# Kernel optimization log

Measured on AMD Instinct MI355X. Metric: run time of the kernel, lower is better.

The kernel has to match this reference:

```python
import jax, jax.numpy as jnp
import numpy as np
from jax import lax

B, L, M, H = 8, 16, 256, 53
HID, NH, HD = 64, 4, 16  # hidden_size, n_heads, head_dim
ACT = 15  # 3 sub-actions x 5 categories


def _lstm_last(x, Wih, Whh, bih, bhh):
    # x: [N, T, D] batch_first; torch LSTM gate order i,f,g,o. Returns last hidden [N, HID].
    N = x.shape[0]
    h0 = jnp.zeros((N, HID), x.dtype)
    c0 = jnp.zeros((N, HID), x.dtype)
    def step(carry, xt):
        h, c = carry
        g = xt @ Wih.T + bih + h @ Whh.T + bhh
        i, f, gg, o = jnp.split(g, 4, axis=-1)
        c = jax.nn.sigmoid(f) * c + jax.nn.sigmoid(i) * jnp.tanh(gg)
        h = jax.nn.sigmoid(o) * jnp.tanh(c)
        return (h, c), None
    (h, _), _ = lax.scan(step, (h0, c0), x.transpose(1, 0, 2))
    return h


def setup_inputs():
    key = jax.random.key(0)
    ks = jax.random.split(key, 32)
    rn = lambda k, sh: (jax.random.normal(k, sh, jnp.float32) * 0.05)
    Gmat = jax.random.randint(ks[3], (M, M), 0, 2)
    Gmat = Gmat.at[jnp.arange(M), jnp.arange(M)].set(1)  # self-contact so no all-masked row
    return {
        'x_actor': jax.random.normal(ks[0], (B, L, M, H), jnp.float32),
        'x_critic': jax.random.normal(ks[1], (B, L, M, H), jnp.float32),
        'action': jax.random.randint(ks[2], (B, M, 3), 0, 5),
        'Gmat': Gmat,
        'Wa': rn(ks[4], (HID, H)), 'ba': jnp.zeros((HID,), jnp.float32),
        'Wg': rn(ks[5], (HID, H)), 'bg': jnp.zeros((HID,), jnp.float32),
        'Qw': rn(ks[6], (HID, HID)), 'Kw': rn(ks[7], (HID, HID)),
        'W2': rn(ks[8], (HID, 2 * HID)), 'b2': jnp.zeros((HID,), jnp.float32),
        'Wih_a': rn(ks[9], (4 * HID, HID)), 'Whh_a': rn(ks[10], (4 * HID, HID)),
        'bih_a': jnp.zeros((4 * HID,), jnp.float32), 'bhh_a': jnp.zeros((4 * HID,), jnp.float32),
        'Wih_c': rn(ks[11], (4 * HID, HID)), 'Whh_c': rn(ks[12], (4 * HID, HID)),
        'bih_c': jnp.zeros((4 * HID,), jnp.float32), 'bhh_c': jnp.zeros((4 * HID,), jnp.float32),
        'Wma1': rn(ks[13], (HID, HID)), 'bma1': jnp.zeros((HID,), jnp.float32),
        'Wma2': rn(ks[14], (ACT, HID)), 'bma2': jnp.zeros((ACT,), jnp.float32),
        'Wmc1': rn(ks[15], (HID, HID)), 'bmc1': jnp.zeros((HID,), jnp.float32),
        'Wmc2': rn(ks[16], (1, HID)), 'bmc2': jnp.zeros((1,), jnp.float32),
    }


def reference(x_actor, x_critic, action, Gmat, Wa, ba, Wg, bg, Qw, Kw, W2, b2,
              Wih_a, Whh_a, bih_a, bhh_a, Wih_c, Whh_c, bih_c, bhh_c,
              Wma1, bma1, Wma2, bma2, Wmc1, bmc1, Wmc2, bmc2):
    Bb, Ll, Mm, Hh = x_actor.shape
    xa = x_actor.transpose(1, 0, 2, 3).reshape(Ll * Bb, Mm, Hh)
    xc = xa  # original code overwrites x_critic with x_actor (preserved)
    a_lin = xa @ Wa.T + ba                               # [LB, M, HID]
    # --- GAT (GCN2) ---
    s = xc @ Wg.T + bg                                   # [LB, M, HID]
    q = (s @ Qw).reshape(-1, Mm, NH, HD)
    k = (s @ Kw).reshape(-1, Mm, NH, HD)
    s4 = s.reshape(-1, Mm, NH, HD)
    att = jnp.einsum('blhe,bshe->bhls', q, k) / jnp.asarray(128.0, s.dtype) ** 0.5
    att = jnp.where(Gmat > 0, att, jnp.asarray(-9e15, att.dtype))
    att = jax.nn.softmax(att, axis=-1)
    s_out = jnp.einsum('bshe,bhls->blhe', s4, att).reshape(-1, Mm, NH * HD)
    c_feat = jnp.concatenate([s, s_out], axis=-1) @ W2.T + b2  # [LB, M, HID]
    # --- to sequences [B*M, L, HID] ---
    xa_seq = a_lin.reshape(Ll, Bb * Mm, HID).transpose(1, 0, 2)
    xc_seq = c_feat.reshape(Ll, Bb * Mm, HID).transpose(1, 0, 2)
    ah = _lstm_last(xa_seq, Wih_a, Whh_a, bih_a, bhh_a)          # [B*M, HID]
    ch = _lstm_last(xc_seq, Wih_c, Whh_c, bih_c, bhh_c).reshape(Bb, Mm, HID)
    logits = (jnp.tanh(ah @ Wma1.T + bma1) @ Wma2.T + bma2).reshape(Bb, Mm, 3, 5)
    logp = jax.nn.log_softmax(logits, axis=-1)
    lp = jnp.take_along_axis(logp, action[..., None], axis=-1).squeeze(-1)  # [B,M,3]
    ent = -jnp.sum(jnp.exp(logp) * logp, axis=-1)                           # [B,M,3]
    value = jnp.tanh(ch @ Wmc1.T + bmc1) @ Wmc2.T + bmc2                    # [B,M,1]
    return (action, lp.sum(-1), ent.sum(-1), value)
```

## Files before the change

### kernel.cpp

```cpp
#include <hip/hip_runtime.h>
#include <math.h>

#define B_ 8
#define L_ 16
#define M_ 256
#define H_ 53
#define HID_ 64
#define LB_ 128

typedef __attribute__((ext_vector_type(8))) short bf16x8;
typedef __attribute__((ext_vector_type(4))) float f32x4;

__device__ inline unsigned short f2bf(float f) {
  unsigned u = __builtin_bit_cast(unsigned, f);
  unsigned r = (u + 0x7FFFu + ((u >> 16) & 1u)) >> 16;
  return (unsigned short)r;
}
__device__ inline float sigm(float x) { return __builtin_amdgcn_rcpf(1.f + __expf(-x)); }
__device__ inline float ftanh(float x) { return 1.f - 2.f * __builtin_amdgcn_rcpf(1.f + __expf(2.f * x)); }

__global__ __launch_bounds__(256) void kA_lin(const float* __restrict__ x,
    const float* __restrict__ Wa, const float* __restrict__ ba,
    const float* __restrict__ Wg, const float* __restrict__ bg,
    const float* __restrict__ Qw, const float* __restrict__ Kw,
    const int* __restrict__ Gmat, const float* __restrict__ Wih_c,
    const float* __restrict__ W2, const float* __restrict__ b2,
    unsigned short* __restrict__ a_lin_bf, unsigned short* __restrict__ s_b,
    unsigned short* __restrict__ q_b, unsigned short* __restrict__ k_b,
    unsigned short* __restrict__ sT_b, unsigned short* __restrict__ Wfold_b,
    float* __restrict__ bias_fold, unsigned* __restrict__ gmask) {
  __shared__ float wa_lds[HID_ * H_];
  __shared__ float wg_lds[HID_ * H_];
  __shared__ float x_lds[16][H_];
  __shared__ float s_sh[16][HID_];
  int tid = threadIdx.x;
  int row0 = blockIdx.x * 16;
  int lbA = row0 >> 8, mA0 = row0 & 255;
  for (int i = tid; i < HID_ * H_; i += 256) { wa_lds[i] = Wa[i]; wg_lds[i] = Wg[i]; }
  for (int i = tid; i < 16 * H_; i += 256) {
    int r = i / H_, j = i - r * H_;
    int row = row0 + r;
    int lb = row >> 8, m = row & 255;
    int l = lb >> 3, b = lb & 7;
    x_lds[r][j] = x[((b * L_ + l) * M_ + m) * H_ + j];
  }
  __syncthreads();
  int lane = tid & 63, wv = tid >> 6;
  float aA[4], aS[4];
  float bav = ba[lane], bgv = bg[lane];
  #pragma unroll
  for (int ri = 0; ri < 4; ++ri) { aA[ri] = bav; aS[ri] = bgv; }
  for (int j = 0; j < H_; ++j) {
    float wa = wa_lds[lane * H_ + j];
    float wg = wg_lds[lane * H_ + j];
    #pragma unroll
    for (int ri = 0; ri < 4; ++ri) {
      float xv = x_lds[wv * 4 + ri][j];
      aA[ri] = fmaf(xv, wa, aA[ri]);
      aS[ri] = fmaf(xv, wg, aS[ri]);
    }
  }
  #pragma unroll
  for (int ri = 0; ri < 4; ++ri) {
    int row = row0 + wv * 4 + ri;
    a_lin_bf[row * HID_ + lane] = f2bf(aA[ri]);
    s_sh[wv * 4 + ri][lane] = aS[ri];
    s_b[row * HID_ + lane] = f2bf(aS[ri]);
  }
  __syncthreads();
  {
    int e = tid >> 2, m4 = tid & 3;
    ushort4 v;
    v.x = f2bf(s_sh[m4 * 4 + 0][e]);
    v.y = f2bf(s_sh[m4 * 4 + 1][e]);
    v.z = f2bf(s_sh[m4 * 4 + 2][e]);
    v.w = f2bf(s_sh[m4 * 4 + 3][e]);
    *(ushort4*)&sT_b[(lbA * 64 + e) * 256 + mA0 + m4 * 4] = v;
  }
  float aq[4] = {0.f, 0.f, 0.f, 0.f}, ak[4] = {0.f, 0.f, 0.f, 0.f};
  for (int j = 0; j < HID_; ++j) {
    float qw = Qw[j * HID_ + lane];
    float kw = Kw[j * HID_ + lane];
    #pragma unroll
    for (int ri = 0; ri < 4; ++ri) {
      float sv = s_sh[wv * 4 + ri][j];
      aq[ri] = fmaf(sv, qw, aq[ri]);
      ak[ri] = fmaf(sv, kw, ak[ri]);
    }
  }
  #pragma unroll
  for (int ri = 0; ri < 4; ++ri) {
    int row = row0 + wv * 4 + ri;
    q_b[row * HID_ + lane] = f2bf(aq[ri] * 0.08838834764831845f);
    k_b[row * HID_ + lane] = f2bf(ak[ri]);
  }
  if (blockIdx.x < 256) {
    int l = blockIdx.x;
    int gv = Gmat[l * 256 + tid];
    unsigned long long msk = __ballot(gv > 0);
    if ((tid & 63) == 0) {
      gmask[l * 8 + (tid >> 6) * 2] = (unsigned)msk;
      gmask[l * 8 + (tid >> 6) * 2 + 1] = (unsigned)(msk >> 32);
    }
  } else if (blockIdx.x < 512) {
    int n = blockIdx.x - 256;
    if (tid < 128) {
      float acc = 0.f;
      for (int e = 0; e < 64; ++e) acc = fmaf(Wih_c[n * 64 + e], W2[e * 128 + tid], acc);
      Wfold_b[n * 128 + tid] = f2bf(acc);
      if (tid == 0) {
        float bacc = 0.f;
        for (int e = 0; e < 64; ++e) bacc = fmaf(Wih_c[n * 64 + e], b2[e], bacc);
        bias_fold[n] = bacc;
      }
    }
  }
}

__global__ __launch_bounds__(512, 4) void kB_attn(
    const unsigned short* __restrict__ qb, const unsigned short* __restrict__ kb,
    const unsigned short* __restrict__ sT, const unsigned* __restrict__ gmask,
    unsigned short* __restrict__ so_b) {
  int blk = blockIdx.x;
  int lb = blk >> 2;
  int l0 = (blk & 3) << 6;
  int tid = threadIdx.x;
  int lane = tid & 63, w = tid >> 6;
  int c16 = lane & 15, q4 = lane >> 4;
  int lrow0 = (w >> 1) * 16;
  int h0 = (w & 1) * 2;
  int lrow = lb * 256 + l0 + lrow0;
  int kbase = lb * 256;
  const bf16x8 z8 = {0, 0, 0, 0, 0, 0, 0, 0};
  bf16x8 bq[2];
  #pragma unroll
  for (int hp = 0; hp < 2; ++hp) {
    int h = h0 + hp;
    bq[hp] = (q4 < 2) ? *(const bf16x8*)(qb + (lrow + c16) * 64 + h * 16 + q4 * 8) : z8;
  }
  unsigned gwv[8];
  #pragma unroll
  for (int sp = 0; sp < 8; ++sp) gwv[sp] = gmask[(l0 + lrow0 + c16) * 8 + sp];
  f32x4 accO[2];
  float sumh[2];
  #pragma unroll
  for (int hp = 0; hp < 2; ++hp) { accO[hp] = (f32x4){0.f, 0.f, 0.f, 0.f}; sumh[hp] = 0.f; }

  #pragma unroll
  for (int sp = 0; sp < 8; ++sp) {
    unsigned gw = gwv[sp];
    #pragma unroll
    for (int hp = 0; hp < 2; ++hp) {
      int h = h0 + hp;
      unsigned pk0A, pk1A, pk0B, pk1B;
      #pragma unroll
      for (int tp = 0; tp < 2; ++tp) {
        int t = sp * 2 + tp;
        bf16x8 ka = z8;
        if (q4 < 2) ka = *(const bf16x8*)(kb + (kbase + t * 16 + c16) * 64 + h * 16 + q4 * 8);
        f32x4 d = __builtin_amdgcn_mfma_f32_16x16x32_bf16(ka, bq[hp], (f32x4){0.f, 0.f, 0.f, 0.f}, 0, 0, 0);
        int bitbase = tp * 16 + q4 * 4;
        float p0 = ((gw >> (bitbase + 0)) & 1u) ? __expf(d[0]) : 0.f;
        float p1 = ((gw >> (bitbase + 1)) & 1u) ? __expf(d[1]) : 0.f;
        float p2 = ((gw >> (bitbase + 2)) & 1u) ? __expf(d[2]) : 0.f;
        float p3 = ((gw >> (bitbase + 3)) & 1u) ? __expf(d[3]) : 0.f;
        sumh[hp] += (p0 + p1) + (p2 + p3);
        unsigned lo = (unsigned)f2bf(p0) | ((unsigned)f2bf(p1) << 16);
        unsigned hi = (unsigned)f2bf(p2) | ((unsigned)f2bf(p3) << 16);
        if (tp == 0) { pk0A = lo; pk1A = hi; } else { pk0B = lo; pk1B = hi; }
      }
      int srcA = ((q4 & 1) * 2) * 16 + c16, srcB = srcA + 16;
      unsigned g0A = (unsigned)__shfl((int)pk0A, srcA);
      unsigned g1A = (unsigned)__shfl((int)pk1A, srcA);
      unsigned g2A = (unsigned)__shfl((int)pk0A, srcB);
      unsigned g3A = (unsigned)__shfl((int)pk1A, srcB);
      unsigned g0B = (unsigned)__shfl((int)pk0B, srcA);
      unsigned g1B = (unsigned)__shfl((int)pk1B, srcA);
      unsigned g2B = (unsigned)__shfl((int)pk0B, srcB);
      unsigned g3B = (unsigned)__shfl((int)pk1B, srcB);
      bool useB = (q4 >= 2);
      uint4 av;
      av.x = useB ? g0B : g0A;
      av.y = useB ? g1B : g1A;
      av.z = useB ? g2B : g2A;
      av.w = useB ? g3B : g3A;
      bf16x8 af = __builtin_bit_cast(bf16x8, av);
      bf16x8 bs = *(const bf16x8*)(sT + (lb * 64 + h * 16 + c16) * 256 + sp * 32 + q4 * 8);
      accO[hp] = __builtin_amdgcn_mfma_f32_16x16x32_bf16(af, bs, accO[hp], 0, 0, 0);
    }
  }
  #pragma unroll
  for (int hp = 0; hp < 2; ++hp) {
    int h = h0 + hp;
    float s = sumh[hp];
    s += __shfl_xor(s, 16);
    s += __shfl_xor(s, 32);
    #pragma unroll
    for (int r = 0; r < 4; ++r) {
      float sv = __shfl(s, q4 * 4 + r);
      float o = accO[hp][r] / sv;
      so_b[(lb * 256 + l0 + lrow0 + q4 * 4 + r) * 64 + h * 16 + c16] = f2bf(o);
    }
  }
}

__global__ __launch_bounds__(256, 1) void kR_lstm(
    const unsigned short* __restrict__ a_lin_bf,
    const unsigned short* __restrict__ s_b, const unsigned short* __restrict__ so_b,
    const unsigned short* __restrict__ Wfold_b, const float* __restrict__ bias_fold,
    const float* __restrict__ Wih_a,
    const float* __restrict__ Whh_a, const float* __restrict__ Whh_c,
    const float* __restrict__ bih_a, const float* __restrict__ bhh_a,
    const float* __restrict__ bih_c, const float* __restrict__ bhh_c,
    const int* __restrict__ action,
    const float* __restrict__ Wma1, const float* __restrict__ bma1,
    const float* __restrict__ Wma2, const float* __restrict__ bma2,
    const float* __restrict__ Wmc1, const float* __restrict__ bmc1,
    const float* __restrict__ Wmc2, const float* __restrict__ bmc2,
    float* __restrict__ out) {
  int blk = blockIdx.x;
  int which = blk >> 7, g = blk & 127;
  int seq0 = g * 16;
  int b = seq0 >> 8, m0 = seq0 & 255;
  __shared__ __attribute__((aligned(16))) unsigned short h_lds[2][16][72];
  __shared__ __attribute__((aligned(16))) unsigned short ha_lds[16][72];
  __shared__ float logit_lds[16][16];
  __shared__ float grp_lds[16][8];
  __shared__ float val_lds[16][4];
  int tid = threadIdx.x;
  int lane = tid & 63, w = tid >> 6;
  int c16 = lane & 15, q4 = lane >> 4;
  int hs0 = w * 16;
  const float* Whh = which ? Whh_c : Whh_a;
  const float* bih = which ? bih_c : bih_a;
  const float* bhh = which ? bhh_c : bhh_a;
  bf16x8 bwhh[4][2];
  float bias[4];
  #pragma unroll
  for (int nt = 0; nt < 4; ++nt) {
    int n = nt * 64 + hs0 + c16;
    bias[nt] = bih[n] + bhh[n] + (which ? bias_fold[n] : 0.f);
    #pragma unroll
    for (int kf = 0; kf < 2; ++kf) {
      const float* wp = Whh + n * 64 + kf * 32 + q4 * 8;
      bf16x8 bb;
      #pragma unroll
      for (int j = 0; j < 8; ++j) bb[j] = (short)f2bf(wp[j]);
      bwhh[nt][kf] = bb;
    }
  }
  for (int i = tid; i < 576; i += 256) ((unsigned*)h_lds)[i] = 0u;
  float cr[4] = {0.f, 0.f, 0.f, 0.f};
  const int STEP = 2048 * 64;
  __syncthreads();
  int cur = 0;
  if (which == 0) {
    bf16x8 bwin[4][2];
    #pragma unroll
    for (int nt = 0; nt < 4; ++nt) {
      int n = nt * 64 + hs0 + c16;
      #pragma unroll
      for (int kf = 0; kf < 2; ++kf) {
        const float* wp = Wih_a + n * 64 + kf * 32 + q4 * 8;
        bf16x8 bb;
        #pragma unroll
        for (int j = 0; j < 8; ++j) bb[j] = (short)f2bf(wp[j]);
        bwin[nt][kf] = bb;
      }
    }
    const unsigned short* inb = a_lin_bf + (b * 256 + m0 + c16) * 64;
    bf16x8 i0c = *(const bf16x8*)(inb + q4 * 8);
    bf16x8 i1c = *(const bf16x8*)(inb + 32 + q4 * 8);
    for (int l = 0; l < L_; ++l) {
      bf16x8 i0n = i0c, i1n = i1c;
      if (l < L_ - 1) {
        i0n = *(const bf16x8*)(inb + (l + 1) * STEP + q4 * 8);
        i1n = *(const bf16x8*)(inb + (l + 1) * STEP + 32 + q4 * 8);
      }
      bf16x8 ah0 = *(const bf16x8*)&h_lds[cur][c16][q4 * 8];
      bf16x8 ah1 = *(const bf16x8*)&h_lds[cur][c16][32 + q4 * 8];
      f32x4 acc[4];
      #pragma unroll
      for (int nt = 0; nt < 4; ++nt) {
        f32x4 a = {bias[nt], bias[nt], bias[nt], bias[nt]};
        a = __builtin_amdgcn_mfma_f32_16x16x32_bf16(i0c, bwin[nt][0], a, 0, 0, 0);
        a = __builtin_amdgcn_mfma_f32_16x16x32_bf16(i1c, bwin[nt][1], a, 0, 0, 0);
        a = __builtin_amdgcn_mfma_f32_16x16x32_bf16(ah0, bwhh[nt][0], a, 0, 0, 0);
        a = __builtin_amdgcn_mfma_f32_16x16x32_bf16(ah1, bwhh[nt][1], a, 0, 0, 0);
        acc[nt] = a;
      }
      #pragma unroll
      for (int rr = 0; rr < 4; ++rr) {
        float si = sigm(acc[0][rr]);
        float sf = sigm(acc[1][rr]);
        float gg = ftanh(acc[2][rr]);
        float so_ = sigm(acc[3][rr]);
        cr[rr] = sf * cr[rr] + si * gg;
        float hvv = so_ * ftanh(cr[rr]);
        h_lds[cur ^ 1][q4 * 4 + rr][hs0 + c16] = f2bf(hvv);
      }
      __syncthreads();
      cur ^= 1;
      i0c = i0n; i1c = i1n;
    }
  } else {
    bf16x8 bwf[4][4];
    #pragma unroll
    for (int nt = 0; nt < 4; ++nt) {
      int n = nt * 64 + hs0 + c16;
      #pragma unroll
      for (int kc = 0; kc < 4; ++kc) {
        bwf[nt][kc] = *(const bf16x8*)(Wfold_b + n * 128 + kc * 32 + q4 * 8);
      }
    }
    const unsigned short* sbB = s_b + (b * 256 + m0 + c16) * 64;
    const unsigned short* soB = so_b + (b * 256 + m0 + c16) * 64;
    bf16x8 s0c = *(const bf16x8*)(sbB + q4 * 8);
    bf16x8 s1c = *(const bf16x8*)(sbB + 32 + q4 * 8);
    bf16x8 o0c = *(const bf16x8*)(soB + q4 * 8);
    bf16x8 o1c = *(const bf16x8*)(soB + 32 + q4 * 8);
    for (int l = 0; l < L_; ++l) {
      bf16x8 s0n = s0c, s1n = s1c, o0n = o0c, o1n = o1c;
      if (l < L_ - 1) {
        s0n = *(const bf16x8*)(sbB + (l + 1) * STEP + q4 * 8);
        s1n = *(const bf16x8*)(sbB + (l + 1) * STEP + 32 + q4 * 8);
        o0n = *(const bf16x8*)(soB + (l + 1) * STEP + q4 * 8);
        o1n = *(const bf16x8*)(soB + (l + 1) * STEP + 32 + q4 * 8);
      }
      bf16x8 ah0 = *(const bf16x8*)&h_lds[cur][c16][q4 * 8];
      bf16x8 ah1 = *(const bf16x8*)&h_lds[cur][c16][32 + q4 * 8];
      f32x4 acc[4];
      #pragma unroll
      for (int nt = 0; nt < 4; ++nt) {
        f32x4 a = {bias[nt], bias[nt], bias[nt], bias[nt]};
        a = __builtin_amdgcn_mfma_f32_16x16x32_bf16(s0c, bwf[nt][0], a, 0, 0, 0);
        a = __builtin_amdgcn_mfma_f32_16x16x32_bf16(s1c, bwf[nt][1], a, 0, 0, 0);
        a = __builtin_amdgcn_mfma_f32_16x16x32_bf16(o0c, bwf[nt][2], a, 0, 0, 0);
        a = __builtin_amdgcn_mfma_f32_16x16x32_bf16(o1c, bwf[nt][3], a, 0, 0, 0);
        a = __builtin_amdgcn_mfma_f32_16x16x32_bf16(ah0, bwhh[nt][0], a, 0, 0, 0);
        a = __builtin_amdgcn_mfma_f32_16x16x32_bf16(ah1, bwhh[nt][1], a, 0, 0, 0);
        acc[nt] = a;
      }
      #pragma unroll
      for (int rr = 0; rr < 4; ++rr) {
        float si = sigm(acc[0][rr]);
        float sf = sigm(acc[1][rr]);
        float gg = ftanh(acc[2][rr]);
        float so_ = sigm(acc[3][rr]);
        cr[rr] = sf * cr[rr] + si * gg;
        float hvv = so_ * ftanh(cr[rr]);
        h_lds[cur ^ 1][q4 * 4 + rr][hs0 + c16] = f2bf(hvv);
      }
      __syncthreads();
      cur ^= 1;
      s0c = s0n; s1c = s1n; o0c = o0n; o1c = o1n;
    }
  }
  bf16x8 fh0 = *(const bf16x8*)&h_lds[cur][c16][q4 * 8];
  bf16x8 fh1 = *(const bf16x8*)&h_lds[cur][c16][32 + q4 * 8];
  if (which == 0) {
    bf16x8 bm1[2];
    #pragma unroll
    for (int kf = 0; kf < 2; ++kf) {
      const float* wp = Wma1 + (hs0 + c16) * 64 + kf * 32 + q4 * 8;
      bf16x8 bb;
      #pragma unroll
      for (int j = 0; j < 8; ++j) bb[j] = (short)f2bf(wp[j]);
      bm1[kf] = bb;
    }
    float bs = bma1[hs0 + c16];
    f32x4 acc = {bs, bs, bs, bs};
    acc = __builtin_amdgcn_mfma_f32_16x16x32_bf16(fh0, bm1[0], acc, 0, 0, 0);
    acc = __builtin_amdgcn_mfma_f32_16x16x32_bf16(fh1, bm1[1], acc, 0, 0, 0);
    #pragma unroll
    for (int rr = 0; rr < 4; ++rr)
      ha_lds[q4 * 4 + rr][hs0 + c16] = f2bf(ftanh(acc[rr]));
    __syncthreads();
    if (w == 0) {
      bf16x8 af0 = *(const bf16x8*)&ha_lds[c16][q4 * 8];
      bf16x8 af1 = *(const bf16x8*)&ha_lds[c16][32 + q4 * 8];
      const bf16x8 z8 = {0, 0, 0, 0, 0, 0, 0, 0};
      bf16x8 bw2[2] = {z8, z8};
      float bs2 = 0.f;
      if (c16 < 15) {
        #pragma unroll
        for (int kf = 0; kf < 2; ++kf) {
          const float* wp = Wma2 + c16 * 64 + kf * 32 + q4 * 8;
          bf16x8 bb;
          #pragma unroll
          for (int j = 0; j < 8; ++j) bb[j] = (short)f2bf(wp[j]);
          bw2[kf] = bb;
        }
        bs2 = bma2[c16];
      }
      f32x4 acc2 = {bs2, bs2, bs2, bs2};
      acc2 = __builtin_amdgcn_mfma_f32_16x16x32_bf16(af0, bw2[0], acc2, 0, 0, 0);
      acc2 = __builtin_amdgcn_mfma_f32_16x16x32_bf16(af1, bw2[1], acc2, 0, 0, 0);
      #pragma unroll
      for (int rr = 0; rr < 4; ++rr)
        logit_lds[q4 * 4 + rr][c16] = acc2[rr];
    }
    __syncthreads();
    if (tid < 48) {
      int useq = tid & 15, t = tid >> 4;
      int n = seq0 + useq;
      float l0 = logit_lds[useq][t * 5 + 0], l1 = logit_lds[useq][t * 5 + 1];
      float l2 = logit_lds[useq][t * 5 + 2], l3 = logit_lds[useq][t * 5 + 3];
      float l4 = logit_lds[useq][t * 5 + 4];
      float mx = fmaxf(fmaxf(fmaxf(l0, l1), fmaxf(l2, l3)), l4);
      float sm = __expf(l0 - mx) + __expf(l1 - mx) + __expf(l2 - mx) +
                 __expf(l3 - mx) + __expf(l4 - mx);
      float lse = __logf(sm) + mx;
      int a = action[n * 3 + t];
      float lp0 = l0 - lse, lp1 = l1 - lse, lp2 = l2 - lse, lp3 = l3 - lse, lp4 = l4 - lse;
      float lpsel = logit_lds[useq][t * 5 + a] - lse;
      float ent = -(__expf(lp0) * lp0 + __expf(lp1) * lp1 + __expf(lp2) * lp2 +
                    __expf(lp3) * lp3 + __expf(lp4) * lp4);
      grp_lds[useq][t] = lpsel;
      grp_lds[useq][4 + t] = ent;
      out[n * 3 + t] = (float)a;
    }
    __syncthreads();
    if (tid < 16) {
      int n = seq0 + tid;
      out[6144 + n] = grp_lds[tid][0] + grp_lds[tid][1] + grp_lds[tid][2];
      out[8192 + n] = grp_lds[tid][4] + grp_lds[tid][5] + grp_lds[tid][6];
    }
  } else {
    bf16x8 bm1[2];
    #pragma unroll
    for (int kf = 0; kf < 2; ++kf) {
      const float* wp = Wmc1 + (hs0 + c16) * 64 + kf * 32 + q4 * 8;
      bf16x8 bb;
      #pragma unroll
      for (int j = 0; j < 8; ++j) bb[j] = (short)f2bf(wp[j]);
      bm1[kf] = bb;
    }
    float bs = bmc1[hs0 + c16];
    f32x4 acc = {bs, bs, bs, bs};
    acc = __builtin_amdgcn_mfma_f32_16x16x32_bf16(fh0, bm1[0], acc, 0, 0, 0);
    acc = __builtin_amdgcn_mfma_f32_16x16x32_bf16(fh1, bm1[1], acc, 0, 0, 0);
    float wv2 = Wmc2[hs0 + c16];
    float pv[4];
    #pragma unroll
    for (int rr = 0; rr < 4; ++rr) pv[rr] = ftanh(acc[rr]) * wv2;
    #pragma unroll
    for (int rr = 0; rr < 4; ++rr) {
      pv[rr] += __shfl_xor(pv[rr], 1);
      pv[rr] += __shfl_xor(pv[rr], 2);
      pv[rr] += __shfl_xor(pv[rr], 4);
      pv[rr] += __shfl_xor(pv[rr], 8);
    }
    if (c16 == 0) {
      #pragma unroll
      for (int rr = 0; rr < 4; ++rr) val_lds[q4 * 4 + rr][w] = pv[rr];
    }
    __syncthreads();
    if (tid < 16) {
      int n = seq0 + tid;
      out[10240 + n] = val_lds[tid][0] + val_lds[tid][1] + val_lds[tid][2] +
                       val_lds[tid][3] + bmc2[0];
    }
  }
}

extern "C" void kernel_launch(void* const* d_in, const int* in_sizes, int n_in,
                              void* d_out, int out_size, void* d_ws, size_t ws_size,
                              hipStream_t stream) {
  const float* x_actor = (const float*)d_in[0];
  const int* action = (const int*)d_in[2];
  const int* Gmat  = (const int*)d_in[3];
  const float* Wa = (const float*)d_in[4];  const float* ba = (const float*)d_in[5];
  const float* Wg = (const float*)d_in[6];  const float* bg = (const float*)d_in[7];
  const float* Qw = (const float*)d_in[8];  const float* Kw = (const float*)d_in[9];
  const float* W2 = (const float*)d_in[10]; const float* b2 = (const float*)d_in[11];
  const float* Wih_a = (const float*)d_in[12]; const float* Whh_a = (const float*)d_in[13];
  const float* bih_a = (const float*)d_in[14]; const float* bhh_a = (const float*)d_in[15];
  const float* Wih_c = (const float*)d_in[16]; const float* Whh_c = (const float*)d_in[17];
  const float* bih_c = (const float*)d_in[18]; const float* bhh_c = (const float*)d_in[19];
  const float* Wma1 = (const float*)d_in[20]; const float* bma1 = (const float*)d_in[21];
  const float* Wma2 = (const float*)d_in[22]; const float* bma2 = (const float*)d_in[23];
  const float* Wmc1 = (const float*)d_in[24]; const float* bmc1 = (const float*)d_in[25];
  const float* Wmc2 = (const float*)d_in[26]; const float* bmc2 = (const float*)d_in[27];

  unsigned short* us = (unsigned short*)d_ws;
  unsigned short* a_lin_bf = us;
  unsigned short* s_b  = us + 2097152;
  unsigned short* q_b  = us + 4194304;
  unsigned short* k_b  = us + 6291456;
  unsigned short* sT_b = us + 8388608;
  unsigned short* so_b = us + 10485760;
  unsigned short* Wfold_b = us + 12582912;
  float* fb = (float*)(us + 12615680);
  float* bias_fold = fb;
  unsigned* gmask = (unsigned*)(fb + 256);
  float* out = (float*)d_out;

  kA_lin<<<2048, 256, 0, stream>>>(x_actor, Wa, ba, Wg, bg, Qw, Kw,
                                   Gmat, Wih_c, W2, b2,
                                   a_lin_bf, s_b, q_b, k_b, sT_b, Wfold_b,
                                   bias_fold, gmask);
  kB_attn<<<512, 512, 0, stream>>>(q_b, k_b, sT_b, gmask, so_b);
  kR_lstm<<<256, 256, 0, stream>>>(a_lin_bf, s_b, so_b, Wfold_b, bias_fold,
                                   Wih_a, Whh_a, Whh_c, bih_a, bhh_a, bih_c, bhh_c,
                                   action, Wma1, bma1, Wma2, bma2,
                                   Wmc1, bmc1, Wmc2, bmc2, out);
}
```

Measured before the change: 79.41 us.

## Fold Q/K projections into input weights and compute linears with MFMA

Weight-only preprocessing (Wfold, the Q/K-through-Wg fold with its bias, and the Gmat bitmask) moves into a separate small kernel. The main linear kernel then computes a_lin, s, q and k directly from x with bf16 MFMA over 64-row tiles, replacing the scalar FP32 FMA loops. Staged LDS outputs are written out with vectorized stores. This removes the chained s→q/k matmul and the scalar FLOP cost, but adds a kernel launch and extra bf16 rounding of x and the folded weights.

After: 77.65 us. -2.2%, faster.

```diff
diff --git a/kernel.cpp b/kernel.cpp
--- a/kernel.cpp
+++ b/kernel.cpp
@@ -7,6 +7,7 @@
 #define H_ 53
 #define HID_ 64
 #define LB_ 128
+#define SCALE_ 0.08838834764831845f
 
 typedef __attribute__((ext_vector_type(8))) short bf16x8;
 typedef __attribute__((ext_vector_type(4))) float f32x4;
@@ -19,101 +20,132 @@
 __device__ inline float sigm(float x) { return __builtin_amdgcn_rcpf(1.f + __expf(-x)); }
 __device__ inline float ftanh(float x) { return 1.f - 2.f * __builtin_amdgcn_rcpf(1.f + __expf(2.f * x)); }
 
-__global__ __launch_bounds__(256) void kA_lin(const float* __restrict__ x,
+__global__ __launch_bounds__(256) void kP_pre(
+    const float* __restrict__ Wg, const float* __restrict__ bg,
+    const float* __restrict__ Qw, const float* __restrict__ Kw,
+    const float* __restrict__ Wih_c, const float* __restrict__ W2,
+    const float* __restrict__ b2, const int* __restrict__ Gmat,
+    unsigned short* __restrict__ WQ_b, unsigned short* __restrict__ WK_b,
+    float* __restrict__ bqk, unsigned short* __restrict__ Wfold_b,
+    float* __restrict__ bias_fold, unsigned* __restrict__ gmask) {
+  int blk = blockIdx.x, tid = threadIdx.x;
+  if (blk < 128) {
+    int idx = blk * 256 + tid;
+    int n = idx >> 7, t = idx & 127;
+    float acc = 0.f;
+    for (int e = 0; e < 64; ++e) acc = fmaf(Wih_c[n * 64 + e], W2[e * 128 + t], acc);
+    Wfold_b[idx] = f2bf(acc);
+  } else if (blk < 160) {
+    int idx = (blk - 128) * 256 + tid;
+    int which = idx >> 12, n = (idx >> 6) & 63, j = idx & 63;
+    const float* Mm = which ? Kw : Qw;
+    float acc = 0.f;
+    if (j < 53) {
+      for (int e = 0; e < 64; ++e) acc = fmaf(Mm[e * 64 + n], Wg[e * 53 + j], acc);
+      if (which == 0) acc *= SCALE_;
+    }
+    (which ? WK_b : WQ_b)[n * 64 + j] = f2bf(acc);
+  } else if (blk == 160) {
+    if (tid < 128) {
+      int which = tid >> 6, n = tid & 63;
+      const float* Mm = which ? Kw : Qw;
+      float acc = 0.f;
+      for (int e = 0; e < 64; ++e) acc = fmaf(bg[e], Mm[e * 64 + n], acc);
+      if (which == 0) acc *= SCALE_;
+      bqk[tid] = acc;
+    }
+  } else if (blk == 161) {
+    float acc = 0.f;
+    for (int e = 0; e < 64; ++e) acc = fmaf(Wih_c[tid * 64 + e], b2[e], acc);
+    bias_fold[tid] = acc;
+  } else {
+    int w = tid >> 6, ln = tid & 63;
+    int l = (blk - 162) * 4 + w;
+    #pragma unroll
+    for (int c = 0; c < 4; ++c) {
+      int gv = Gmat[l * 256 + c * 64 + ln];
+      unsigned long long msk = __ballot(gv > 0);
+      if (ln == 0) {
+        gmask[l * 8 + c * 2] = (unsigned)msk;
+        gmask[l * 8 + c * 2 + 1] = (unsigned)(msk >> 32);
+      }
+    }
+  }
+}
+
+#define XS 68
+#define WS 68
+#define OS 264
+__global__ __launch_bounds__(256, 2) void kA_lin(const float* __restrict__ x,
     const float* __restrict__ Wa, const float* __restrict__ ba,
     const float* __restrict__ Wg, const float* __restrict__ bg,
-    const float* __restrict__ Qw, const float* __restrict__ Kw,
-    const int* __restrict__ Gmat, const float* __restrict__ Wih_c,
-    const float* __restrict__ W2, const float* __restrict__ b2,
+    const unsigned short* __restrict__ WQ_b, const unsigned short* __restrict__ WK_b,
+    const float* __restrict__ bqk,
     unsigned short* __restrict__ a_lin_bf, unsigned short* __restrict__ s_b,
     unsigned short* __restrict__ q_b, unsigned short* __restrict__ k_b,
-    unsigned short* __restrict__ sT_b, unsigned short* __restrict__ Wfold_b,
-    float* __restrict__ bias_fold, unsigned* __restrict__ gmask) {
-  __shared__ float wa_lds[HID_ * H_];
-  __shared__ float wg_lds[HID_ * H_];
-  __shared__ float x_lds[16][H_];
-  __shared__ float s_sh[16][HID_];
+    unsigned short* __restrict__ sT_b) {
+  __shared__ __attribute__((aligned(16))) unsigned short x_lds[64 * XS];
+  __shared__ __attribute__((aligned(16))) unsigned short w_lds[256 * WS];
+  __shared__ float bias_lds[256];
+  __shared__ __attribute__((aligned(16))) unsigned short out_lds[64 * OS];
   int tid = threadIdx.x;
-  int row0 = blockIdx.x * 16;
-  int lbA = row0 >> 8, mA0 = row0 & 255;
-  for (int i = tid; i < HID_ * H_; i += 256) { wa_lds[i] = Wa[i]; wg_lds[i] = Wg[i]; }
-  for (int i = tid; i < 16 * H_; i += 256) {
-    int r = i / H_, j = i - r * H_;
+  int row0 = blockIdx.x * 64;
+  for (int i = tid; i < 64 * 64; i += 256) {
+    int r = i >> 6, j = i & 63;
     int row = row0 + r;
     int lb = row >> 8, m = row & 255;
     int l = lb >> 3, b = lb & 7;
-    x_lds[r][j] = x[((b * L_ + l) * M_ + m) * H_ + j];
+    float v = (j < 53) ? x[((b * L_ + l) * M_ + m) * H_ + j] : 0.f;
+    x_lds[r * XS + j] = f2bf(v);
+  }
+  for (int i = tid; i < 64 * 64; i += 256) {
+    int n = i >> 6, j = i & 63;
+    w_lds[n * WS + j] = (j < 53) ? f2bf(Wa[n * 53 + j]) : 0;
+    w_lds[(64 + n) * WS + j] = (j < 53) ? f2bf(Wg[n * 53 + j]) : 0;
+    w_lds[(128 + n) * WS + j] = WQ_b[i];
+    w_lds[(192 + n) * WS + j] = WK_b[i];
+  }
+  {
+    float bv;
+    if (tid < 64) bv = ba[tid];
+    else if (tid < 128) bv = bg[tid - 64];
+    else bv = bqk[tid - 128];
+    bias_lds[tid] = bv;
   }
   __syncthreads();
-  int lane = tid & 63, wv = tid >> 6;
-  float aA[4], aS[4];
-  float bav = ba[lane], bgv = bg[lane];
-  #pragma unroll
-  for (int ri = 0; ri < 4; ++ri) { aA[ri] = bav; aS[ri] = bgv; }
-  for (int j = 0; j < H_; ++j) {
-    float wa = wa_lds[lane * H_ + j];
-    float wg = wg_lds[lane * H_ + j];
-    #pragma unroll
-    for (int ri = 0; ri < 4; ++ri) {
-      float xv = x_lds[wv * 4 + ri][j];
-      aA[ri] = fmaf(xv, wa, aA[ri]);
-      aS[ri] = fmaf(xv, wg, aS[ri]);
-    }
-  }
-  #pragma unroll
-  for (int ri = 0; ri < 4; ++ri) {
-    int row = row0 + wv * 4 + ri;
-    a_lin_bf[row * HID_ + lane] = f2bf(aA[ri]);
-    s_sh[wv * 4 + ri][lane] = aS[ri];
-    s_b[row * HID_ + lane] = f2bf(aS[ri]);
+  int lane = tid & 63, w = tid >> 6;
+  int c16 = lane & 15, q4 = lane >> 4;
+  bf16x8 a0 = *(const bf16x8*)&x_lds[(w * 16 + c16) * XS + q4 * 8];
+  bf16x8 a1 = *(const bf16x8*)&x_lds[(w * 16 + c16) * XS + 32 + q4 * 8];
+  #pragma unroll
+  for (int nt = 0; nt < 16; ++nt) {
+    bf16x8 b0 = *(const bf16x8*)&w_lds[(nt * 16 + c16) * WS + q4 * 8];
+    bf16x8 b1 = *(const bf16x8*)&w_lds[(nt * 16 + c16) * WS + 32 + q4 * 8];
+    float bs = bias_lds[nt * 16 + c16];
+    f32x4 acc = {bs, bs, bs, bs};
+    acc = __builtin_amdgcn_mfma_f32_16x16x32_bf16(a0, b0, acc, 0, 0, 0);
+    acc = __builtin_amdgcn_mfma_f32_16x16x32_bf16(a1, b1, acc, 0, 0, 0);
+    #pragma unroll
+    for (int rr = 0; rr < 4; ++rr)
+      out_lds[(w * 16 + q4 * 4 + rr) * OS + nt * 16 + c16] = f2bf(acc[rr]);
   }
   __syncthreads();
-  {
-    int e = tid >> 2, m4 = tid & 3;
+  for (int i = tid; i < 2048; i += 256) {
+    int r = i >> 5, seg = i & 31;
+    int which = seg >> 3, n8 = (seg & 7) * 8;
+    uint4 v = *(const uint4*)&out_lds[r * OS + which * 64 + n8];
+    unsigned short* dst = which == 0 ? a_lin_bf : which == 1 ? s_b : which == 2 ? q_b : k_b;
+    *(uint4*)&dst[(row0 + r) * 64 + n8] = v;
+  }
+  int lb = row0 >> 8, m0 = row0 & 255;
+  for (int i = tid; i < 1024; i += 256) {
+    int e = i >> 4, mc = i & 15;
     ushort4 v;
-    v.x = f2bf(s_sh[m4 * 4 + 0][e]);
-    v.y = f2bf(s_sh[m4 * 4 + 1][e]);
-    v.z = f2bf(s_sh[m4 * 4 + 2][e]);
-    v.w = f2bf(s_sh[m4 * 4 + 3][e]);
-    *(ushort4*)&sT_b[(lbA * 64 + e) * 256 + mA0 + m4 * 4] = v;
-  }
-  float aq[4] = {0.f, 0.f, 0.f, 0.f}, ak[4] = {0.f, 0.f, 0.f, 0.f};
-  for (int j = 0; j < HID_; ++j) {
-    float qw = Qw[j * HID_ + lane];
-    float kw = Kw[j * HID_ + lane];
-    #pragma unroll
-    for (int ri = 0; ri < 4; ++ri) {
-      float sv = s_sh[wv * 4 + ri][j];
-      aq[ri] = fmaf(sv, qw, aq[ri]);
-      ak[ri] = fmaf(sv, kw, ak[ri]);
-    }
-  }
-  #pragma unroll
-  for (int ri = 0; ri < 4; ++ri) {
-    int row = row0 + wv * 4 + ri;
-    q_b[row * HID_ + lane] = f2bf(aq[ri] * 0.08838834764831845f);
-    k_b[row * HID_ + lane] = f2bf(ak[ri]);
-  }
-  if (blockIdx.x < 256) {
-    int l = blockIdx.x;
-    int gv = Gmat[l * 256 + tid];
-    unsigned long long msk = __ballot(gv > 0);
-    if ((tid & 63) == 0) {
-      gmask[l * 8 + (tid >> 6) * 2] = (unsigned)msk;
-      gmask[l * 8 + (tid >> 6) * 2 + 1] = (unsigned)(msk >> 32);
-    }
-  } else if (blockIdx.x < 512) {
-    int n = blockIdx.x - 256;
-    if (tid < 128) {
-      float acc = 0.f;
-      for (int e = 0; e < 64; ++e) acc = fmaf(Wih_c[n * 64 + e], W2[e * 128 + tid], acc);
-      Wfold_b[n * 128 + tid] = f2bf(acc);
-      if (tid == 0) {
-        float bacc = 0.f;
-        for (int e = 0; e < 64; ++e) bacc = fmaf(Wih_c[n * 64 + e], b2[e], bacc);
-        bias_fold[n] = bacc;
-      }
-    }
+    v.x = out_lds[(mc * 4 + 0) * OS + 64 + e];
+    v.y = out_lds[(mc * 4 + 1) * OS + 64 + e];
+    v.z = out_lds[(mc * 4 + 2) * OS + 64 + e];
+    v.w = out_lds[(mc * 4 + 3) * OS + 64 + e];
+    *(ushort4*)&sT_b[(lb * 64 + e) * 256 + m0 + mc * 4] = v;
   }
 }
 
@@ -491,15 +523,18 @@
   unsigned short* sT_b = us + 8388608;
   unsigned short* so_b = us + 10485760;
   unsigned short* Wfold_b = us + 12582912;
-  float* fb = (float*)(us + 12615680);
+  unsigned short* WQ_b = us + 12615680;
+  unsigned short* WK_b = us + 12619776;
+  float* fb = (float*)(us + 12623872);
   float* bias_fold = fb;
-  unsigned* gmask = (unsigned*)(fb + 256);
+  float* bqk = fb + 256;
+  unsigned* gmask = (unsigned*)(fb + 384);
   float* out = (float*)d_out;
 
-  kA_lin<<<2048, 256, 0, stream>>>(x_actor, Wa, ba, Wg, bg, Qw, Kw,
-                                   Gmat, Wih_c, W2, b2,
-                                   a_lin_bf, s_b, q_b, k_b, sT_b, Wfold_b,
-                                   bias_fold, gmask);
+  kP_pre<<<226, 256, 0, stream>>>(Wg, bg, Qw, Kw, Wih_c, W2, b2, Gmat,
+                                  WQ_b, WK_b, bqk, Wfold_b, bias_fold, gmask);
+  kA_lin<<<512, 256, 0, stream>>>(x_actor, Wa, ba, Wg, bg, WQ_b, WK_b, bqk,
+                                  a_lin_bf, s_b, q_b, k_b, sT_b);
   kB_attn<<<512, 512, 0, stream>>>(q_b, k_b, sT_b, gmask, so_b);
   kR_lstm<<<256, 256, 0, stream>>>(a_lin_bf, s_b, so_b, Wfold_b, bias_fold,
                                    Wih_a, Whh_a, Whh_c, bih_a, bhh_a, bih_c, bhh_c,
```
